# Kernel tuning notes

Hardware: AMD Instinct MI355X
Metric: run time of the kernel (lower is better)

## Reference

```python
import jax, jax.numpy as jnp
import numpy as np

N_NODES = 10000
N_EDGES = 160000
D_IN = 50
ALPHA = 0.2  # LeakyReLU negative slope


def _xavier(key, shape):
    fan_in, fan_out = shape[0], int(np.prod(shape[1:]))
    limit = float(np.sqrt(6.0 / (fan_in + fan_out)))
    return jax.random.uniform(key, shape, jnp.float32, -limit, limit)


def setup_inputs() -> dict:
    key = jax.random.key(0)
    ks = jax.random.split(key, 8)
    x = jax.random.normal(ks[0], (N_NODES, D_IN), jnp.float32)
    edge_idx = jax.random.randint(ks[1], (2, N_EDGES), 0, N_NODES, jnp.int64)
    # layer 1: 50 -> 4 heads x 256, concat
    W1 = _xavier(ks[2], (D_IN, 4, 256))
    a1 = _xavier(ks[3], (4, 512))  # [H, 2F]: split into a_src, a_dst
    # layer 2: 1024 -> 4 heads x 256, concat
    W2 = _xavier(ks[4], (1024, 4, 256))
    a2 = _xavier(ks[5], (4, 512))
    # layer 3: 1024 -> 6 heads x 121, mean
    W3 = _xavier(ks[6], (1024, 6, 121))
    a3 = _xavier(ks[7], (6, 242))
    return {"x": x, "edge_idx": edge_idx, "W1": W1, "a1": a1,
            "W2": W2, "a2": a2, "W3": W3, "a3": a3}


def gat_layer(h, W, a, src, dst, aggregate):
    """Multi-head GAT layer over an edge list. h:[N,Din], W:[Din,H,F], a:[H,2F]."""
    N = h.shape[0]
    Wh = jnp.einsum('nd,dhf->nhf', h, W)                    # [N, H, F]
    F = Wh.shape[-1]
    att_src = jnp.einsum('nhf,hf->nh', Wh, a[:, :F])         # a^T [Wh_i || .]
    att_dst = jnp.einsum('nhf,hf->nh', Wh, a[:, F:])         # a^T [. || Wh_j]
    logits = jax.nn.leaky_relu(att_src[src] + att_dst[dst], ALPHA)  # [E, H]
    # numerically stable softmax over incoming edges of each destination node
    m = jax.ops.segment_max(logits, dst, num_segments=N)
    e = jnp.exp(logits - m[dst])
    denom = jax.ops.segment_sum(e, dst, num_segments=N)
    coef = e / (denom[dst] + 1e-16)                           # [E, H]
    out = jax.ops.segment_sum(coef[:, :, None] * Wh[src], dst, num_segments=N)
    if aggregate == 'concat':
        return out.reshape(N, -1)
    return out.mean(axis=1)


def reference(x, edge_idx, W1, a1, W2, a2, W3, a3):
    src, dst = edge_idx[0], edge_idx[1]
    h1 = jax.nn.elu(gat_layer(x, W1, a1, src, dst, 'concat'))   # [N, 1024]
    h2 = jax.nn.elu(gat_layer(h1, W2, a2, src, dst, 'concat'))  # [N, 1024]
    h3_in = h1 + h2                                              # residual skip
    return gat_layer(h3_in, W3, a3, src, dst, 'mean')            # [N, 121]
```

## Files before the change

### kernel.cpp

```cpp
#include <hip/hip_runtime.h>
#include <hip/hip_bf16.h>
#include <math.h>

#define NN 10000
#define NE 160000

typedef __attribute__((ext_vector_type(8))) _Float16 f16x8;
typedef __attribute__((ext_vector_type(4))) _Float16 f16x4;
typedef __attribute__((ext_vector_type(4))) float f32x4;

__global__ void count_kernel(const int* __restrict__ dst, int* __restrict__ counts, int E) {
  int e = blockIdx.x * blockDim.x + threadIdx.x;
  if (e < E) atomicAdd(&counts[dst[e]], 1);
}

__global__ __launch_bounds__(1024) void scan_kernel(const int* __restrict__ counts,
                                                    int* __restrict__ row_ptr,
                                                    int* __restrict__ cursor, int N) {
  __shared__ int sums[1024];
  int t = threadIdx.x;
  const int CH = (N + 1023) >> 10;
  int base = t * CH;
  int s = 0;
  for (int i = 0; i < CH; ++i) { int idx = base + i; if (idx < N) s += counts[idx]; }
  sums[t] = s;
  __syncthreads();
  for (int off = 1; off < 1024; off <<= 1) {
    int v = 0;
    if (t >= off) v = sums[t - off];
    __syncthreads();
    if (t >= off) sums[t] += v;
    __syncthreads();
  }
  int run = (t == 0) ? 0 : sums[t - 1];
  for (int i = 0; i < CH; ++i) {
    int idx = base + i;
    if (idx < N) { row_ptr[idx] = run; cursor[idx] = run; run += counts[idx]; }
  }
  if (t == 0) row_ptr[N] = sums[1023];
}

__global__ void scatter_kernel(const int* __restrict__ src, const int* __restrict__ dst,
                               int* __restrict__ cursor, int* __restrict__ ssrc, int E) {
  int e = blockIdx.x * blockDim.x + threadIdx.x;
  if (e < E) {
    int pos = atomicAdd(&cursor[dst[e]], 1);
    ssrc[pos] = src[e];
  }
}

#define SEG0 (NN * 64)
#define SEG1 (1024 * 64)
#define SEG2 (1024 * 1024)
#define SEG3 (768 * 1024)
__global__ void prep_kernel(const float* __restrict__ x, const float* __restrict__ W1,
                            const float* __restrict__ W2, const float* __restrict__ W3,
                            _Float16* __restrict__ xh, _Float16* __restrict__ w1,
                            _Float16* __restrict__ w2, _Float16* __restrict__ w3) {
  int i = blockIdx.x * blockDim.x + threadIdx.x;
  if (i < SEG0) {
    int m = i >> 6, k = i & 63;
    xh[i] = (_Float16)(k < 50 ? x[m * 50 + k] : 0.f);
  } else if (i < SEG0 + SEG1) {
    int j = i - SEG0;
    int n = j >> 6, k = j & 63;
    w1[j] = (_Float16)(k < 50 ? W1[k * 1024 + n] : 0.f);
  } else if (i < SEG0 + SEG1 + SEG2) {
    int j = i - SEG0 - SEG1;
    int n = j >> 10, k = j & 1023;
    w2[j] = (_Float16)W2[k * 1024 + n];
  } else if (i < SEG0 + SEG1 + SEG2 + SEG3) {
    int j = i - SEG0 - SEG1 - SEG2;
    int n = j >> 10, k = j & 1023;
    w3[j] = (_Float16)(n < 726 ? W3[k * 726 + n] : 0.f);
  }
}

template<int PAD121>
__global__ __launch_bounds__(256) void gemm_f16(const _Float16* __restrict__ A,
                                                const _Float16* __restrict__ B,
                                                _Float16* __restrict__ C,
                                                int M, int KP, int NcStore, int NC) {
  int flat = blockIdx.x;
  int xcd = flat & 7;
  int slot = flat >> 3;
  int cblk = slot % NC;
  int rblk = (slot / NC) * 8 + xcd;
  const int m0 = rblk * 128;
  if (m0 >= M) return;
  const int n0 = cblk * 128;

  __shared__ _Float16 As[128 * 72];
  __shared__ _Float16 Bs[128 * 72];

  const int t = threadIdx.x;
  const int lane = t & 63;
  const int wid = t >> 6;
  const int wr = wid >> 1;
  const int wc = wid & 1;
  const int row_in = lane & 15;
  const int kgrp = lane >> 4;

  f32x4 acc[4][4];
#pragma unroll
  for (int i = 0; i < 4; ++i)
#pragma unroll
    for (int j = 0; j < 4; ++j) acc[i][j] = (f32x4){0.f, 0.f, 0.f, 0.f};

  for (int k0 = 0; k0 < KP; k0 += 64) {
    if (k0) __syncthreads();
#pragma unroll
    for (int i = 0; i < 4; ++i) {
      int lin = (i * 256 + t) * 8;
      int row = lin >> 6;
      int k = lin & 63;
      int gm = m0 + row;
      if (gm >= M) gm = M - 1;
      *(f16x8*)&As[row * 72 + k] = *(const f16x8*)&A[(size_t)gm * KP + k0 + k];
      *(f16x8*)&Bs[row * 72 + k] = *(const f16x8*)&B[(size_t)(n0 + row) * KP + k0 + k];
    }
    __syncthreads();

#pragma unroll
    for (int ks = 0; ks < 64; ks += 32) {
      f16x8 a[4], b[4];
#pragma unroll
      for (int mi = 0; mi < 4; ++mi)
        a[mi] = *(const f16x8*)&As[(wr * 64 + mi * 16 + row_in) * 72 + ks + kgrp * 8];
#pragma unroll
      for (int ni = 0; ni < 4; ++ni)
        b[ni] = *(const f16x8*)&Bs[(wc * 64 + ni * 16 + row_in) * 72 + ks + kgrp * 8];
#pragma unroll
      for (int mi = 0; mi < 4; ++mi)
#pragma unroll
        for (int ni = 0; ni < 4; ++ni)
          acc[mi][ni] = __builtin_amdgcn_mfma_f32_16x16x32_f16(a[mi], b[ni], acc[mi][ni], 0, 0, 0);
    }
  }

#pragma unroll
  for (int mi = 0; mi < 4; ++mi) {
#pragma unroll
    for (int ni = 0; ni < 4; ++ni) {
      int gn = n0 + wc * 64 + ni * 16 + row_in;
      if (gn >= NcStore) continue;
#pragma unroll
      for (int j = 0; j < 4; ++j) {
        int gm = m0 + wr * 64 + mi * 16 + kgrp * 4 + j;
        if (gm >= M) continue;
        if (PAD121) {
          int h = gn / 121;
          int pc = h * 128 + (gn - h * 121);
          C[(size_t)gm * 768 + pc] = (_Float16)acc[mi][ni][j];
        } else {
          C[(size_t)gm * NcStore + gn] = (_Float16)acc[mi][ni][j];
        }
      }
    }
  }
}

template<int H, int F, int SW, int HS>
__global__ void att_kernel(const _Float16* __restrict__ Whb, const float* __restrict__ a,
                           float* __restrict__ att_s, float* __restrict__ att_d, int N) {
  int n = blockIdx.x;
  int h = threadIdx.x >> 6;
  int lane = threadIdx.x & 63;
  const _Float16* w = Whb + (size_t)n * SW + h * HS;
  const float* as = a + (size_t)h * 2 * F;
  const float* ad = as + F;
  float ss = 0.f, sd = 0.f;
  for (int f = lane; f < F; f += 64) {
    float v = (float)w[f];
    ss += v * as[f];
    sd += v * ad[f];
  }
#pragma unroll
  for (int off = 32; off > 0; off >>= 1) {
    ss += __shfl_down(ss, off);
    sd += __shfl_down(sd, off);
  }
  if (lane == 0) {
    att_s[n * H + h] = ss;
    att_d[n * H + h] = sd;
  }
}

template<int H>
__global__ __launch_bounds__(64) void edge_softmax_csr(const int* __restrict__ row_ptr,
                                                       const int* __restrict__ ssrc,
                                                       const float* __restrict__ att_s,
                                                       const float* __restrict__ att_d,
                                                       float* __restrict__ cbuf, int N) {
  int n = blockIdx.x;
  int lane = threadIdx.x;
  int beg = row_ptr[n], end = row_ptr[n + 1];
  float ad[H];
#pragma unroll
  for (int h = 0; h < H; ++h) ad[h] = att_d[n * H + h];

  float m[H];
#pragma unroll
  for (int h = 0; h < H; ++h) m[h] = -INFINITY;
  for (int k = beg + lane; k < end; k += 64) {
    int s = ssrc[k];
#pragma unroll
    for (int h = 0; h < H; ++h) {
      float x = att_s[s * H + h] + ad[h];
      float l = x >= 0.f ? x : 0.2f * x;
      m[h] = fmaxf(m[h], l);
    }
  }
#pragma unroll
  for (int h = 0; h < H; ++h)
#pragma unroll
    for (int off = 32; off > 0; off >>= 1) m[h] = fmaxf(m[h], __shfl_xor(m[h], off));

  float sum[H];
#pragma unroll
  for (int h = 0; h < H; ++h) sum[h] = 0.f;
  for (int k = beg + lane; k < end; k += 64) {
    int s = ssrc[k];
#pragma unroll
    for (int h = 0; h < H; ++h) {
      float x = att_s[s * H + h] + ad[h];
      float l = x >= 0.f ? x : 0.2f * x;
      float ev = __expf(l - m[h]);
      cbuf[(size_t)k * H + h] = ev;
      sum[h] += ev;
    }
  }
#pragma unroll
  for (int h = 0; h < H; ++h) {
#pragma unroll
    for (int off = 32; off > 0; off >>= 1) sum[h] += __shfl_xor(sum[h], off);
    sum[h] = 1.f / (sum[h] + 1e-16f);
  }
  for (int k = beg + lane; k < end; k += 64) {
#pragma unroll
    for (int h = 0; h < H; ++h) cbuf[(size_t)k * H + h] *= sum[h];
  }
}

template<int MODE>
__global__ __launch_bounds__(256) void aggregate_cat_chunk(const int* __restrict__ row_ptr,
                                                           const int* __restrict__ ssrc,
                                                           const float* __restrict__ cbuf,
                                                           const _Float16* __restrict__ Whb,
                                                           const _Float16* __restrict__ h1,
                                                           _Float16* __restrict__ outv, int N) {
  int b = blockIdx.x;
  int chunk = b & 7;
  int group = b >> 3;
  int n = group * 16 + (threadIdx.x >> 4);
  if (n >= N) return;
  int tt = threadIdx.x & 15;
  int idx = chunk * 128 + tt * 8;
  int h = chunk >> 1;

  float acc[8] = {};
  int beg = row_ptr[n], end = row_ptr[n + 1];
  int k = beg;
  for (; k + 1 < end; k += 2) {
    int s0 = ssrc[k], s1 = ssrc[k + 1];
    float c0 = cbuf[(size_t)k * 4 + h];
    float c1 = cbuf[(size_t)(k + 1) * 4 + h];
    f16x8 w0 = *(const f16x8*)&Whb[(size_t)s0 * 1024 + idx];
    f16x8 w1 = *(const f16x8*)&Whb[(size_t)s1 * 1024 + idx];
#pragma unroll
    for (int j = 0; j < 8; ++j) {
      acc[j] += c0 * (float)w0[j];
      acc[j] += c1 * (float)w1[j];
    }
  }
  if (k < end) {
    int s0 = ssrc[k];
    float c0 = cbuf[(size_t)k * 4 + h];
    f16x8 w0 = *(const f16x8*)&Whb[(size_t)s0 * 1024 + idx];
#pragma unroll
    for (int j = 0; j < 8; ++j) acc[j] += c0 * (float)w0[j];
  }

  size_t o = (size_t)n * 1024 + idx;
  f16x8 r1;
  if (MODE == 1) r1 = *(const f16x8*)&h1[o];
  f16x8 vo;
#pragma unroll
  for (int j = 0; j < 8; ++j) {
    float v = acc[j];
    v = v > 0.f ? v : expm1f(v);
    if (MODE == 1) v += (float)r1[j];
    vo[j] = (_Float16)v;
  }
  *(f16x8*)&outv[o] = vo;
}

__global__ __launch_bounds__(256) void aggregate_mean_chunk(const int* __restrict__ row_ptr,
                                                            const int* __restrict__ ssrc,
                                                            const float* __restrict__ cbuf,
                                                            const _Float16* __restrict__ Whb,
                                                            float* __restrict__ part, int N) {
  int b = blockIdx.x;
  int h = b & 7;
  if (h >= 6) return;
  int n = (b >> 3) * 16 + (threadIdx.x >> 4);
  if (n >= N) return;
  int tt = threadIdx.x & 15;
  int base = h * 128 + tt * 8;

  float acc[8] = {};
  int beg = row_ptr[n], end = row_ptr[n + 1];
  int k = beg;
  for (; k + 1 < end; k += 2) {
    int s0 = ssrc[k], s1 = ssrc[k + 1];
    float c0 = cbuf[(size_t)k * 6 + h];
    float c1 = cbuf[(size_t)(k + 1) * 6 + h];
    f16x8 w0 = *(const f16x8*)&Whb[(size_t)s0 * 768 + base];
    f16x8 w1 = *(const f16x8*)&Whb[(size_t)s1 * 768 + base];
#pragma unroll
    for (int j = 0; j < 8; ++j) {
      acc[j] += c0 * (float)w0[j];
      acc[j] += c1 * (float)w1[j];
    }
  }
  if (k < end) {
    int s0 = ssrc[k];
    float c0 = cbuf[(size_t)k * 6 + h];
    f16x8 w0 = *(const f16x8*)&Whb[(size_t)s0 * 768 + base];
#pragma unroll
    for (int j = 0; j < 8; ++j) acc[j] += c0 * (float)w0[j];
  }

  float* p = &part[(size_t)n * 768 + base];
  *(f32x4*)&p[0] = (f32x4){acc[0], acc[1], acc[2], acc[3]};
  *(f32x4*)&p[4] = (f32x4){acc[4], acc[5], acc[6], acc[7]};
}

__global__ __launch_bounds__(128) void reduce_mean(const float* __restrict__ part,
                                                   float* __restrict__ out, int N) {
  int n = blockIdx.x;
  int f = threadIdx.x;
  if (f >= 121) return;
  const float* p = &part[(size_t)n * 768];
  float s = 0.f;
#pragma unroll
  for (int h = 0; h < 6; ++h) s += p[h * 128 + f];
  out[(size_t)n * 121 + f] = s * (1.0f / 6.0f);
}

extern "C" void kernel_launch(void* const* d_in, const int* in_sizes, int n_in,
                              void* d_out, int out_size, void* d_ws, size_t ws_size,
                              hipStream_t stream) {
  const float* x  = (const float*)d_in[0];
  const int* eidx = (const int*)d_in[1];
  const float* W1 = (const float*)d_in[2];
  const float* a1 = (const float*)d_in[3];
  const float* W2 = (const float*)d_in[4];
  const float* a2 = (const float*)d_in[5];
  const float* W3 = (const float*)d_in[6];
  const float* a3 = (const float*)d_in[7];
  float* out = (float*)d_out;

  const int N = NN, E = NE;
  const int* src = eidx;
  const int* dst = eidx + E;

  char* ws = (char*)d_ws;
  size_t off = 0;
  auto alloc = [&](size_t bytes) -> void* {
    void* p = ws + off;
    off += (bytes + 255) & ~(size_t)255;
    return p;
  };
  _Float16* Whf  = (_Float16*)alloc((size_t)N * 1024 * 2);
  _Float16* h1   = (_Float16*)alloc((size_t)N * 1024 * 2);
  _Float16* hsum = (_Float16*)alloc((size_t)N * 1024 * 2);
  _Float16* xh   = (_Float16*)alloc((size_t)N * 64 * 2);
  _Float16* w1   = (_Float16*)alloc((size_t)1024 * 64 * 2);
  _Float16* w2   = (_Float16*)alloc((size_t)1024 * 1024 * 2);
  _Float16* w3   = (_Float16*)alloc((size_t)768 * 1024 * 2);
  float* cbuf  = (float*)alloc((size_t)E * 6 * 4);
  float* part  = (float*)alloc((size_t)N * 768 * 4);
  float* atts  = (float*)alloc((size_t)N * 6 * 4);
  float* attd  = (float*)alloc((size_t)N * 6 * 4);
  int* counts  = (int*)alloc((size_t)N * 4);
  int* row_ptr = (int*)alloc((size_t)(N + 1) * 4);
  int* cursor  = (int*)alloc((size_t)N * 4);
  int* ssrc    = (int*)alloc((size_t)E * 4);

  hipMemsetAsync(counts, 0, (size_t)N * 4, stream);
  prep_kernel<<<(SEG0 + SEG1 + SEG2 + SEG3 + 255) / 256, 256, 0, stream>>>(x, W1, W2, W3, xh, w1, w2, w3);
  count_kernel<<<(E + 255) / 256, 256, 0, stream>>>(dst, counts, E);
  scan_kernel<<<1, 1024, 0, stream>>>(counts, row_ptr, cursor, N);
  scatter_kernel<<<(E + 255) / 256, 256, 0, stream>>>(src, dst, cursor, ssrc, E);

  const int RPG = 10;
  const int AGG_GRID = 8 * ((N + 15) / 16);

  gemm_f16<0><<<8 * RPG * 8, 256, 0, stream>>>(xh, w1, Whf, N, 64, 1024, 8);
  att_kernel<4, 256, 1024, 256><<<N, 256, 0, stream>>>(Whf, a1, atts, attd, N);
  edge_softmax_csr<4><<<N, 64, 0, stream>>>(row_ptr, ssrc, atts, attd, cbuf, N);
  aggregate_cat_chunk<0><<<AGG_GRID, 256, 0, stream>>>(row_ptr, ssrc, cbuf, Whf, nullptr, h1, N);

  gemm_f16<0><<<8 * RPG * 8, 256, 0, stream>>>(h1, w2, Whf, N, 1024, 1024, 8);
  att_kernel<4, 256, 1024, 256><<<N, 256, 0, stream>>>(Whf, a2, atts, attd, N);
  edge_softmax_csr<4><<<N, 64, 0, stream>>>(row_ptr, ssrc, atts, attd, cbuf, N);
  aggregate_cat_chunk<1><<<AGG_GRID, 256, 0, stream>>>(row_ptr, ssrc, cbuf, Whf, h1, hsum, N);

  gemm_f16<1><<<8 * RPG * 6, 256, 0, stream>>>(hsum, w3, Whf, N, 1024, 726, 6);
  att_kernel<6, 121, 768, 128><<<N, 384, 0, stream>>>(Whf, a3, atts, attd, N);
  edge_softmax_csr<6><<<N, 64, 0, stream>>>(row_ptr, ssrc, atts, attd, cbuf, N);
  aggregate_mean_chunk<<<AGG_GRID, 256, 0, stream>>>(row_ptr, ssrc, cbuf, Whf, part, N);
  reduce_mean<<<N, 128, 0, stream>>>(part, out, N);
}
```

Baseline: 299.2 us.

## Fold attention projections into GEMM weights and defer softmax normalization

Precomputes W·a_src and W·a_dst vectors and appends them as extra output columns of each layer's weight matrix, so the GEMM produces attention logits directly and the separate att_kernel launches go away. The softmax kernel no longer rescales cbuf in a third pass; it stores per-node reciprocal denominators that the aggregation kernels apply at the end. Edge counting is merged into the prep kernel. This costs an extra 128-column GEMM tile per layer and computes the attention dot products in fp16 from precomputed weights, which changes rounding slightly.

```diff
diff --git a/kernel.cpp b/kernel.cpp
--- a/kernel.cpp
+++ b/kernel.cpp
@@ -8,11 +8,6 @@
 typedef __attribute__((ext_vector_type(8))) _Float16 f16x8;
 typedef __attribute__((ext_vector_type(4))) _Float16 f16x4;
 typedef __attribute__((ext_vector_type(4))) float f32x4;
-
-__global__ void count_kernel(const int* __restrict__ dst, int* __restrict__ counts, int E) {
-  int e = blockIdx.x * blockDim.x + threadIdx.x;
-  if (e < E) atomicAdd(&counts[dst[e]], 1);
-}
 
 __global__ __launch_bounds__(1024) void scan_kernel(const int* __restrict__ counts,
                                                     int* __restrict__ row_ptr,
@@ -49,38 +44,111 @@
   }
 }
 
-#define SEG0 (NN * 64)
-#define SEG1 (1024 * 64)
-#define SEG2 (1024 * 1024)
-#define SEG3 (768 * 1024)
-__global__ void prep_kernel(const float* __restrict__ x, const float* __restrict__ W1,
-                            const float* __restrict__ W2, const float* __restrict__ W3,
-                            _Float16* __restrict__ xh, _Float16* __restrict__ w1,
-                            _Float16* __restrict__ w2, _Float16* __restrict__ w3) {
+#define P0 (NN * 64)
+#define P1 (1024 * 64)
+#define P1B (128 * 64)
+#define P2 (1024 * 1024)
+#define P2B (128 * 1024)
+#define P3 (768 * 1024)
+#define P3B (128 * 1024)
+#define P4 NE
+__global__ void prep_kernel(const float* __restrict__ x,
+                            const float* __restrict__ W1, const float* __restrict__ a1,
+                            const float* __restrict__ W2, const float* __restrict__ a2,
+                            const float* __restrict__ W3, const float* __restrict__ a3,
+                            const int* __restrict__ dst, int* __restrict__ counts,
+                            _Float16* __restrict__ xh, _Float16* __restrict__ w1p,
+                            _Float16* __restrict__ w2p, _Float16* __restrict__ w3p) {
   int i = blockIdx.x * blockDim.x + threadIdx.x;
-  if (i < SEG0) {
+  if (i < P0) {
     int m = i >> 6, k = i & 63;
     xh[i] = (_Float16)(k < 50 ? x[m * 50 + k] : 0.f);
-  } else if (i < SEG0 + SEG1) {
-    int j = i - SEG0;
-    int n = j >> 6, k = j & 63;
-    w1[j] = (_Float16)(k < 50 ? W1[k * 1024 + n] : 0.f);
-  } else if (i < SEG0 + SEG1 + SEG2) {
-    int j = i - SEG0 - SEG1;
-    int n = j >> 10, k = j & 1023;
-    w2[j] = (_Float16)W2[k * 1024 + n];
-  } else if (i < SEG0 + SEG1 + SEG2 + SEG3) {
-    int j = i - SEG0 - SEG1 - SEG2;
-    int n = j >> 10, k = j & 1023;
-    w3[j] = (_Float16)(n < 726 ? W3[k * 726 + n] : 0.f);
-  }
-}
-
-template<int PAD121>
+    return;
+  }
+  i -= P0;
+  if (i < P1) {
+    int n = i >> 6, k = i & 63;
+    w1p[i] = (_Float16)(k < 50 ? W1[k * 1024 + n] : 0.f);
+    return;
+  }
+  i -= P1;
+  if (i < P1B) {
+    int j = i >> 6, k = i & 63;
+    float v = 0.f;
+    if (j < 8 && k < 50) {
+      int h = j & 3, side = j >> 2;
+      const float* wp = W1 + k * 1024 + h * 256;
+      const float* ap = a1 + h * 512 + side * 256;
+      float s = 0.f;
+      for (int f = 0; f < 256; f += 4) {
+        f32x4 wv = *(const f32x4*)&wp[f];
+        f32x4 av = *(const f32x4*)&ap[f];
+        s += wv.x * av.x + wv.y * av.y + wv.z * av.z + wv.w * av.w;
+      }
+      v = s;
+    }
+    w1p[(1024 + j) * 64 + k] = (_Float16)v;
+    return;
+  }
+  i -= P1B;
+  if (i < P2) {
+    int n = i >> 10, k = i & 1023;
+    w2p[i] = (_Float16)W2[k * 1024 + n];
+    return;
+  }
+  i -= P2;
+  if (i < P2B) {
+    int j = i >> 10, k = i & 1023;
+    float v = 0.f;
+    if (j < 8) {
+      int h = j & 3, side = j >> 2;
+      const float* wp = W2 + k * 1024 + h * 256;
+      const float* ap = a2 + h * 512 + side * 256;
+      float s = 0.f;
+      for (int f = 0; f < 256; f += 4) {
+        f32x4 wv = *(const f32x4*)&wp[f];
+        f32x4 av = *(const f32x4*)&ap[f];
+        s += wv.x * av.x + wv.y * av.y + wv.z * av.z + wv.w * av.w;
+      }
+      v = s;
+    }
+    w2p[(1024 + j) * 1024 + k] = (_Float16)v;
+    return;
+  }
+  i -= P2B;
+  if (i < P3) {
+    int n = i >> 10, k = i & 1023;
+    w3p[i] = (_Float16)(n < 726 ? W3[k * 726 + n] : 0.f);
+    return;
+  }
+  i -= P3;
+  if (i < P3B) {
+    int j = i >> 10, k = i & 1023;
+    float v = 0.f;
+    if (j < 12) {
+      int h = (j < 6) ? j : j - 6;
+      int side = (j < 6) ? 0 : 1;
+      const float* wp = W3 + k * 726 + h * 121;
+      const float* ap = a3 + h * 242 + side * 121;
+      float s = 0.f;
+#pragma unroll 11
+      for (int f = 0; f < 121; ++f) s += wp[f] * ap[f];
+      v = s;
+    }
+    w3p[(768 + j) * 1024 + k] = (_Float16)v;
+    return;
+  }
+  i -= P3B;
+  if (i < P4) atomicAdd(&counts[dst[i]], 1);
+}
+
+template<int PAD121, int HH>
 __global__ __launch_bounds__(256) void gemm_f16(const _Float16* __restrict__ A,
                                                 const _Float16* __restrict__ B,
                                                 _Float16* __restrict__ C,
-                                                int M, int KP, int NcStore, int NC) {
+                                                float* __restrict__ atts,
+                                                float* __restrict__ attd,
+                                                int M, int KP, int NC) {
   int flat = blockIdx.x;
   int xcd = flat & 7;
   int slot = flat >> 3;
@@ -138,51 +206,38 @@
     }
   }
 
+  constexpr int ATTBASE = PAD121 ? 768 : 1024;
 #pragma unroll
   for (int mi = 0; mi < 4; ++mi) {
 #pragma unroll
     for (int ni = 0; ni < 4; ++ni) {
       int gn = n0 + wc * 64 + ni * 16 + row_in;
-      if (gn >= NcStore) continue;
 #pragma unroll
       for (int j = 0; j < 4; ++j) {
         int gm = m0 + wr * 64 + mi * 16 + kgrp * 4 + j;
         if (gm >= M) continue;
+        float v = acc[mi][ni][j];
         if (PAD121) {
-          int h = gn / 121;
-          int pc = h * 128 + (gn - h * 121);
-          C[(size_t)gm * 768 + pc] = (_Float16)acc[mi][ni][j];
+          if (gn < 726) {
+            int h = gn / 121;
+            int pc = h * 128 + (gn - h * 121);
+            C[(size_t)gm * 768 + pc] = (_Float16)v;
+          } else if (gn >= ATTBASE && gn < ATTBASE + HH) {
+            atts[(size_t)gm * HH + gn - ATTBASE] = v;
+          } else if (gn >= ATTBASE + HH && gn < ATTBASE + 2 * HH) {
+            attd[(size_t)gm * HH + gn - ATTBASE - HH] = v;
+          }
         } else {
-          C[(size_t)gm * NcStore + gn] = (_Float16)acc[mi][ni][j];
+          if (gn < 1024) {
+            C[(size_t)gm * 1024 + gn] = (_Float16)v;
+          } else if (gn < 1024 + HH) {
+            atts[(size_t)gm * HH + gn - 1024] = v;
+          } else if (gn < 1024 + 2 * HH) {
+            attd[(size_t)gm * HH + gn - 1024 - HH] = v;
+          }
         }
       }
     }
-  }
-}
-
-template<int H, int F, int SW, int HS>
-__global__ void att_kernel(const _Float16* __restrict__ Whb, const float* __restrict__ a,
-                           float* __restrict__ att_s, float* __restrict__ att_d, int N) {
-  int n = blockIdx.x;
-  int h = threadIdx.x >> 6;
-  int lane = threadIdx.x & 63;
-  const _Float16* w = Whb + (size_t)n * SW + h * HS;
-  const float* as = a + (size_t)h * 2 * F;
-  const float* ad = as + F;
-  float ss = 0.f, sd = 0.f;
-  for (int f = lane; f < F; f += 64) {
-    float v = (float)w[f];
-    ss += v * as[f];
-    sd += v * ad[f];
-  }
-#pragma unroll
-  for (int off = 32; off > 0; off >>= 1) {
-    ss += __shfl_down(ss, off);
-    sd += __shfl_down(sd, off);
-  }
-  if (lane == 0) {
-    att_s[n * H + h] = ss;
-    att_d[n * H + h] = sd;
   }
 }
 
@@ -191,7 +246,8 @@
                                                        const int* __restrict__ ssrc,
                                                        const float* __restrict__ att_s,
                                                        const float* __restrict__ att_d,
-                                                       float* __restrict__ cbuf, int N) {
+                                                       float* __restrict__ cbuf,
+                                                       float* __restrict__ dinv, int N) {
   int n = blockIdx.x;
   int lane = threadIdx.x;
   int beg = row_ptr[n], end = row_ptr[n + 1];
@@ -234,18 +290,15 @@
   for (int h = 0; h < H; ++h) {
 #pragma unroll
     for (int off = 32; off > 0; off >>= 1) sum[h] += __shfl_xor(sum[h], off);
-    sum[h] = 1.f / (sum[h] + 1e-16f);
-  }
-  for (int k = beg + lane; k < end; k += 64) {
-#pragma unroll
-    for (int h = 0; h < H; ++h) cbuf[(size_t)k * H + h] *= sum[h];
-  }
+  }
+  if (lane < H) dinv[n * H + lane] = 1.f / (sum[lane] + 1e-16f);
 }
 
 template<int MODE>
 __global__ __launch_bounds__(256) void aggregate_cat_chunk(const int* __restrict__ row_ptr,
                                                            const int* __restrict__ ssrc,
                                                            const float* __restrict__ cbuf,
+                                                           const float* __restrict__ dinv,
                                                            const _Float16* __restrict__ Whb,
                                                            const _Float16* __restrict__ h1,
                                                            _Float16* __restrict__ outv, int N) {
@@ -257,6 +310,7 @@
   int tt = threadIdx.x & 15;
   int idx = chunk * 128 + tt * 8;
   int h = chunk >> 1;
+  float inv = dinv[n * 4 + h];
 
   float acc[8] = {};
   int beg = row_ptr[n], end = row_ptr[n + 1];
@@ -287,7 +341,7 @@
   f16x8 vo;
 #pragma unroll
   for (int j = 0; j < 8; ++j) {
-    float v = acc[j];
+    float v = acc[j] * inv;
     v = v > 0.f ? v : expm1f(v);
     if (MODE == 1) v += (float)r1[j];
     vo[j] = (_Float16)v;
@@ -298,6 +352,7 @@
 __global__ __launch_bounds__(256) void aggregate_mean_chunk(const int* __restrict__ row_ptr,
                                                             const int* __restrict__ ssrc,
                                                             const float* __restrict__ cbuf,
+                                                            const float* __restrict__ dinv,
                                                             const _Float16* __restrict__ Whb,
                                                             float* __restrict__ part, int N) {
   int b = blockIdx.x;
@@ -307,6 +362,7 @@
   if (n >= N) return;
   int tt = threadIdx.x & 15;
   int base = h * 128 + tt * 8;
+  float inv = dinv[n * 6 + h];
 
   float acc[8] = {};
   int beg = row_ptr[n], end = row_ptr[n + 1];
@@ -332,8 +388,8 @@
   }
 
   float* p = &part[(size_t)n * 768 + base];
-  *(f32x4*)&p[0] = (f32x4){acc[0], acc[1], acc[2], acc[3]};
-  *(f32x4*)&p[4] = (f32x4){acc[4], acc[5], acc[6], acc[7]};
+  *(f32x4*)&p[0] = (f32x4){acc[0] * inv, acc[1] * inv, acc[2] * inv, acc[3] * inv};
+  *(f32x4*)&p[4] = (f32x4){acc[4] * inv, acc[5] * inv, acc[6] * inv, acc[7] * inv};
 }
 
 __global__ __launch_bounds__(128) void reduce_mean(const float* __restrict__ part,
@@ -376,40 +432,39 @@
   _Float16* h1   = (_Float16*)alloc((size_t)N * 1024 * 2);
   _Float16* hsum = (_Float16*)alloc((size_t)N * 1024 * 2);
   _Float16* xh   = (_Float16*)alloc((size_t)N * 64 * 2);
-  _Float16* w1   = (_Float16*)alloc((size_t)1024 * 64 * 2);
-  _Float16* w2   = (_Float16*)alloc((size_t)1024 * 1024 * 2);
-  _Float16* w3   = (_Float16*)alloc((size_t)768 * 1024 * 2);
+  _Float16* w1p  = (_Float16*)alloc((size_t)1152 * 64 * 2);
+  _Float16* w2p  = (_Float16*)alloc((size_t)1152 * 1024 * 2);
+  _Float16* w3p  = (_Float16*)alloc((size_t)896 * 1024 * 2);
   float* cbuf  = (float*)alloc((size_t)E * 6 * 4);
   float* part  = (float*)alloc((size_t)N * 768 * 4);
   float* atts  = (float*)alloc((size_t)N * 6 * 4);
   float* attd  = (float*)alloc((size_t)N * 6 * 4);
+  float* dinv  = (float*)alloc((size_t)N * 6 * 4);
   int* counts  = (int*)alloc((size_t)N * 4);
   int* row_ptr = (int*)alloc((size_t)(N + 1) * 4);
   int* cursor  = (int*)alloc((size_t)N * 4);
   int* ssrc    = (int*)alloc((size_t)E * 4);
 
   hipMemsetAsync(counts, 0, (size_t)N * 4, stream);
-  prep_kernel<<<(SEG0 + SEG1 + SEG2 + SEG3 + 255) / 256, 256, 0, stream>>>(x, W1, W2, W3, xh, w1, w2, w3);
-  count_kernel<<<(E + 255) / 256, 256, 0, stream>>>(dst, counts, E);
+  const int PTOT = P0 + P1 + P1B + P2 + P2B + P3 + P3B + P4;
+  prep_kernel<<<(PTOT + 255) / 256, 256, 0, stream>>>(x, W1, a1, W2, a2, W3, a3,
+                                                      dst, counts, xh, w1p, w2p, w3p);
   scan_kernel<<<1, 1024, 0, stream>>>(counts, row_ptr, cursor, N);
   scatter_kernel<<<(E + 255) / 256, 256, 0, stream>>>(src, dst, cursor, ssrc, E);
 
   const int RPG = 10;
   const int AGG_GRID = 8 * ((N + 15) / 16);
 
-  gemm_f16<0><<<8 * RPG * 8, 256, 0, stream>>>(xh, w1, Whf, N, 64, 1024, 8);
-  att_kernel<4, 256, 1024, 256><<<N, 256, 0, stream>>>(Whf, a1, atts, attd, N);
-  edge_softmax_csr<4><<<N, 64, 0, stream>>>(row_ptr, ssrc, atts, attd, cbuf, N);
-  aggregate_cat_chunk<0><<<AGG_GRID, 256, 0, stream>>>(row_ptr, ssrc, cbuf, Whf, nullptr, h1, N);
-
-  gemm_f16<0><<<8 * RPG * 8, 256, 0, stream>>>(h1, w2, Whf, N, 1024, 1024, 8);
-  att_kernel<4, 256, 1024, 256><<<N, 256, 0, stream>>>(Whf, a2, atts, attd, N);
-  edge_softmax_csr<4><<<N, 64, 0, stream>>>(row_ptr, ssrc, atts, attd, cbuf, N);
-  aggregate_cat_chunk<1><<<AGG_GRID, 256, 0, stream>>>(row_ptr, ssrc, cbuf, Whf, h1, hsum, N);
-
-  gemm_f16<1><<<8 * RPG * 6, 256, 0, stream>>>(hsum, w3, Whf, N, 1024, 726, 6);
-  att_kernel<6, 121, 768, 128><<<N, 384, 0, stream>>>(Whf, a3, atts, attd, N);
-  edge_softmax_csr<6><<<N, 64, 0, stream>>>(row_ptr, ssrc, atts, attd, cbuf, N);
-  aggregate_mean_chunk<<<AGG_GRID, 256, 0, stream>>>(row_ptr, ssrc, cbuf, Whf, part, N);
+  gemm_f16<0, 4><<<8 * RPG * 9, 256, 0, stream>>>(xh, w1p, Whf, atts, attd, N, 64, 9);
+  edge_softmax_csr<4><<<N, 64, 0, stream>>>(row_ptr, ssrc, atts, attd, cbuf, dinv, N);
+  aggregate_cat_chunk<0><<<AGG_GRID, 256, 0, stream>>>(row_ptr, ssrc, cbuf, dinv, Whf, nullptr, h1, N);
+
+  gemm_f16<0, 4><<<8 * RPG * 9, 256, 0, stream>>>(h1, w2p, Whf, atts, attd, N, 1024, 9);
+  edge_softmax_csr<4><<<N, 64, 0, stream>>>(row_ptr, ssrc, atts, attd, cbuf, dinv, N);
+  aggregate_cat_chunk<1><<<AGG_GRID, 256, 0, stream>>>(row_ptr, ssrc, cbuf, dinv, Whf, h1, hsum, N);
+
+  gemm_f16<1, 6><<<8 * RPG * 7, 256, 0, stream>>>(hsum, w3p, Whf, atts, attd, N, 1024, 7);
+  edge_softmax_csr<6><<<N, 64, 0, stream>>>(row_ptr, ssrc, atts, attd, cbuf, dinv, N);
+  aggregate_mean_chunk<<<AGG_GRID, 256, 0, stream>>>(row_ptr, ssrc, cbuf, dinv, Whf, part, N);
   reduce_mean<<<N, 128, 0, stream>>>(part, out, N);
 }
```

New measurement: 301.1 us. No clear change (+0.6%).
